# Kernel optimization log

Hardware: AMD Instinct MI355X
Metric: run time of the kernel (lower is better)

Reference implementation:

```python
import jax, jax.numpy as jnp
import numpy as np

WS = 2048            # window_size
STEP = WS // 2       # hop = window_size // 2
NC = WS // 2 + 1     # rfft coeffs
NB = 4               # n_blocks


def _hann():
    # periodic hann window (torch.hann_window default)
    return 0.5 - 0.5 * jnp.cos(2.0 * jnp.pi * jnp.arange(WS) / WS)


def _block(x, transfer, gain):
    # x: (b, 1, time); transfer: (NC,); gain: scalar
    b, ch, time = x.shape
    frames = time // STEP
    padded = jnp.pad(x, ((0, 0), (0, 0), (0, STEP)))
    idx = jnp.arange(frames)[:, None] * STEP + jnp.arange(WS)[None, :]
    windowed = padded[:, :, idx]                       # (b, ch, F, WS)
    spec = jnp.fft.rfft(windowed, axis=-1)             # (b, ch, F, NC) complex
    spec_t = jnp.moveaxis(spec, 2, 0)                  # (F, b, ch, NC)
    tc = transfer.astype(spec.dtype)

    # linear recurrence: out_i = transfer * (spec_i + out_{i-1})
    def step_fn(carry, s):
        out = (s + carry) * tc
        return out, out

    _, outs = jax.lax.scan(step_fn, jnp.zeros_like(spec_t[0]), spec_t)
    wins = jnp.fft.irfft(outs, n=WS, axis=-1) * _hann()  # (F, b, ch, WS)
    wins = jnp.moveaxis(wins, 0, 2)                      # (b, ch, F, WS)
    # overlap-add with hop = WS/2: split each frame into two halves
    first = wins[..., :STEP].reshape(b, ch, frames * STEP)
    second = wins[..., STEP:].reshape(b, ch, frames * STEP)
    samples = (jnp.pad(first, ((0, 0), (0, 0), (0, STEP)))
               + jnp.pad(second, ((0, 0), (0, 0), (STEP, 0))))
    return jnp.tanh(samples * gain)[..., :time]


def setup_inputs() -> dict:
    key = jax.random.key(0)
    k_x, k_b, k_s, k_g = jax.random.split(key, 4)
    x = jax.random.normal(k_x, (32, 1, 262144), dtype=jnp.float32)
    # init_transfer: sparse resonances * scaling * pitch^2
    resonances = (jax.random.uniform(k_b, (NB, NC)) < 0.01).astype(jnp.float32)
    scaling = jax.random.uniform(k_s, (NB, NC), minval=0.9, maxval=0.998)
    pitch = jnp.linspace(1.0, 0.0, NC) ** 2
    transfers = resonances * scaling * pitch[None, :]
    gains = jax.random.uniform(k_g, (NB,), minval=10.0, maxval=200.0)
    mixer = jnp.zeros((NB + 1,), dtype=jnp.float32)
    return {"x": x, "transfers": transfers, "gains": gains, "mixer": mixer}


def reference(x, transfers, gains, mixer):
    outputs = [x]
    inp = x
    for i in range(NB):
        inp = _block(inp, transfers[i], gains[i])
        outputs.append(inp)
    stacked = jnp.stack(outputs, axis=-1)          # (b, 1, time, NB+1)
    mixer_values = jax.nn.softmax(mixer)
    return jnp.sum(stacked * mixer_values, axis=-1)
```

## Files before the change

kernel.cpp:

```cpp
#include <hip/hip_runtime.h>
#include <math.h>
#include <stdint.h>

#define NB   4
#define NC   1025
#define WSZ  2048
#define STEP 1024
#define FRM  256
#define BAT  32
#define TT   262144
#define KC   32
#define YPAD 68

#define RREV (1.0f / 2048.0f)

typedef float f2 __attribute__((ext_vector_type(2)));

__device__ __forceinline__ float tanh_fast(float z) {
    float e = __expf(2.0f * z);
    return 1.0f - 2.0f / (e + 1.0f);
}

__device__ __forceinline__ void cis_rev(int idx, float* c, float* s) {
    float rev = (float)(idx & 2047) * RREV;
    *c = __builtin_amdgcn_cosf(rev);
    *s = __builtin_amdgcn_sinf(rev);
}

__global__ __launch_bounds__(1024) void setup_kernel(
    const float* __restrict__ transfers, const float* __restrict__ mixer,
    int* __restrict__ counts, int* __restrict__ bins, float* __restrict__ tvals,
    float* __restrict__ wmix, float* __restrict__ hann, int kmax)
{
    int i = blockIdx.x, tid = threadIdx.x;
    __shared__ int wcnt[16], woff[16];
    if (i == 0) {
        float cc, ss; cis_rev(tid, &cc, &ss);
        hann[tid] = 0.5f - 0.5f * cc;
    }
    float tv = transfers[i * NC + tid];
    bool nz = (tv != 0.0f);
    unsigned long long mask = __ballot(nz);
    int lane = tid & 63, w = tid >> 6;
    int within = __popcll(mask & ((1ULL << lane) - 1ULL));
    if (lane == 0) wcnt[w] = __popcll(mask);
    __syncthreads();
    if (tid == 0) {
        int acc = 0;
        for (int q = 0; q < 16; ++q) { woff[q] = acc; acc += wcnt[q]; }
        float tvL = transfers[i * NC + 1024];
        if (tvL != 0.0f && acc < kmax) { bins[i * NC + acc] = 1024; tvals[i * NC + acc] = tvL; acc++; }
        counts[i] = (acc < kmax) ? acc : kmax;
        if (i == 0) {
            float m = mixer[0];
            for (int q = 1; q < 5; ++q) m = fmaxf(m, mixer[q]);
            float e[5], s = 0.f;
            for (int q = 0; q < 5; ++q) { e[q] = __expf(mixer[q] - m); s += e[q]; }
            for (int q = 0; q < 5; ++q) wmix[q] = e[q] / s;
        }
    }
    __syncthreads();
    if (nz) {
        int pos = woff[w] + within;
        if (pos < kmax) { bins[i * NC + pos] = tid; tvals[i * NC + pos] = tv; }
    }
}

__global__ __launch_bounds__(256) void table_kernel(
    const int* __restrict__ counts, const int* __restrict__ bins,
    float2* __restrict__ cisA, float2* __restrict__ cisB, int kmax)
{
    int i = blockIdx.x >> 2, c = blockIdx.x & 3;
    int K = counts[i];
    int tid = threadIdx.x;
    for (int j = c; j < K; j += 4) {
        int k = bins[i * NC + j];
        if (tid < 64) {
            float cc, ss; cis_rev(k * tid, &cc, &ss);
            cisA[((size_t)i * kmax + j) * 64 + tid] = make_float2(cc, ss);
        } else if (tid < 80) {
            int q = tid - 64;
            float cc, ss; cis_rev(k * 64 * q, &cc, &ss);
            cisB[((size_t)i * kmax + j) * 16 + q] = make_float2(cc, ss);
        }
    }
}

__device__ __forceinline__ void half_dft(
    const float xr[16], int K, const float2* __restrict__ cA,
    const float2* __restrict__ cB, float2* __restrict__ Hout, int lane, int w)
{
    for (int j = w; j < K; j += 8) {
        int j2 = j + 4;
        bool two = (j2 < K);
        float2 bA = cB[(size_t)j * 16 + 1];
        float2 bB = two ? cB[(size_t)j2 * 16 + 1] : bA;
        float2 wAl = cA[(size_t)j * 64 + lane];
        float2 wBl = two ? cA[(size_t)j2 * 64 + lane] : wAl;
        f2 Wr, Wi, nWi;
        Wr.x = bA.x; Wr.y = bB.x;
        Wi.x = -bA.y; Wi.y = -bB.y;
        nWi = -Wi;
        f2 hr = 0.f, hi = 0.f;
#pragma unroll
        for (int i = 15; i >= 0; --i) {
            f2 xx; xx.x = xr[i]; xx.y = xr[i];
            f2 tmp = nWi * hi + xx;
            f2 nr = Wr * hr + tmp;
            hi = Wi * hr + Wr * hi;
            hr = nr;
        }
        f2 wlc, wls;
        wlc.x = wAl.x; wlc.y = wBl.x;
        wls.x = wAl.y; wls.y = wBl.y;
        f2 re = hr * wlc + hi * wls;
        f2 im = hi * wlc - hr * wls;
        float reA = re.x, imA = im.x, reB = re.y, imB = im.y;
#pragma unroll
        for (int m = 32; m >= 1; m >>= 1) {
            reA += __shfl_xor(reA, m, 64);
            imA += __shfl_xor(imA, m, 64);
            reB += __shfl_xor(reB, m, 64);
            imB += __shfl_xor(imB, m, 64);
        }
        if (lane == 0) {
            Hout[j] = make_float2(reA, imA);
            if (two) Hout[j2] = make_float2(reB, imB);
        }
    }
}

__global__ __launch_bounds__(256, 8) void analysis_kernel(
    const float* __restrict__ x, const int* __restrict__ counts,
    const float2* __restrict__ cisA, const float2* __restrict__ cisB,
    float2* __restrict__ H, int iblk, int kmax)
{
    int wg = blockIdx.x;
    int b = wg >> 8, h = wg & 255;
    int tid = threadIdx.x;
    int lane = tid & 63, w = tid >> 6;
    int K = counts[iblk];
    const float* xb = x + (size_t)b * TT + (size_t)h * STEP;
    float xr[16];
#pragma unroll
    for (int i = 0; i < 16; ++i) xr[i] = xb[lane + (i << 6)];
    const float2* cA = cisA + (size_t)iblk * kmax * 64;
    const float2* cB = cisB + (size_t)iblk * kmax * 16;
    float2* Hout = H + (size_t)(b * FRM + h) * K;
    half_dft(xr, K, cA, cB, Hout, lane, w);
}

__global__ __launch_bounds__(256) void scan_kernel(
    float2* __restrict__ S, const int* __restrict__ counts,
    const int* __restrict__ bins, const float* __restrict__ tvals, int iblk)
{
    int K = counts[iblk];
    int wg = blockIdx.x;
    int b = wg & (BAT - 1), j0 = wg >> 5;
    int f = threadIdx.x;
    int lane = f & 63, w = f >> 6;
    __shared__ float2 wtot[4];
    for (int j = j0; j < K; j += 32) {
        float t = tvals[iblk * NC + j];
        int k = bins[iblk * NC + j];
        float2* Sb = S + (size_t)b * FRM * K + j;
        float2 h1 = Sb[(size_t)f * K];
        float2 h2 = (f < FRM - 1) ? Sb[(size_t)(f + 1) * K] : make_float2(0.f, 0.f);
        float sgn = (k & 1) ? -t : t;
        float ax = fmaf(sgn, h2.x, h1.x * t);
        float ay = fmaf(sgn, h2.y, h1.y * t);
        float td = t;
        float tp0, tp1, tp2, tp3, tp4, tp5;
#pragma unroll
        for (int s = 0; s < 6; ++s) {
            int d = 1 << s;
            if (s == 0) tp0 = td; else if (s == 1) tp1 = td; else if (s == 2) tp2 = td;
            else if (s == 3) tp3 = td; else if (s == 4) tp4 = td; else tp5 = td;
            float bx = __shfl_up(ax, d, 64);
            float by = __shfl_up(ay, d, 64);
            if (lane >= d) { ax = fmaf(td, bx, ax); ay = fmaf(td, by, ay); }
            td *= td;
        }
        if (lane == 63) wtot[w] = make_float2(ax, ay);
        __syncthreads();
        float px = 0.f, py = 0.f;
#pragma unroll
        for (int w2 = 0; w2 < 3; ++w2) {
            if (w2 < w) {
                float2 v = wtot[w2];
                px = fmaf(px, td, v.x);
                py = fmaf(py, td, v.y);
            }
        }
        int n = lane + 1;
        float fac = (n & 64) ? td : 1.0f;
        if (n & 1)  fac *= tp0;
        if (n & 2)  fac *= tp1;
        if (n & 4)  fac *= tp2;
        if (n & 8)  fac *= tp3;
        if (n & 16) fac *= tp4;
        if (n & 32) fac *= tp5;
        ax = fmaf(fac, px, ax);
        ay = fmaf(fac, py, ay);
        Sb[(size_t)f * K] = make_float2(ax, ay);
        __syncthreads();
    }
}

__device__ __forceinline__ void acc4(
    f2& q0, f2& q1, f2& q2, f2& q3, float4 e, float4 a0, float4 a1)
{
    f2 up; up.x = e.x; up.y = e.y;
    f2 vp; vp.x = e.z; vp.y = e.w;
    q0 = up * a0.x + q0; q0 = vp * a0.y + q0;
    q1 = up * a0.z + q1; q1 = vp * a0.w + q1;
    q2 = up * a1.x + q2; q2 = vp * a1.y + q2;
    q3 = up * a1.z + q3; q3 = vp * a1.w + q3;
}

__global__ __launch_bounds__(256, 6) void fused_synth_kernel(
    const float2* __restrict__ S, float2* __restrict__ H2,
    const float2* __restrict__ cisA, const float2* __restrict__ cisB,
    const int* __restrict__ counts, const int* __restrict__ bins,
    const float* __restrict__ gains, const float* __restrict__ wmix,
    const float* __restrict__ hann, const float* __restrict__ x,
    float* __restrict__ dout, int iblk, int do_an, int kmax)
{
    __shared__ float4 smem[1024];
    float4* rc = smem;
    float*  ystage = (float*)smem;
    float4* part = smem + 544;

    int wg = blockIdx.x;
    int b = wg >> 7, s0 = (wg & 127) << 1;
    int tid = threadIdx.x;
    int n1 = tid << 2;
    int q = tid >> 4;
    int m = (tid & 15) << 2;

    int K = counts[iblk];
    const int* bl = bins + iblk * NC;
    const float2* Ob = S + (size_t)b * FRM * K;
    const float2* cA0 = cisA + (size_t)iblk * kmax * 64;
    const float2* cB0 = cisB + (size_t)iblk * kmax * 16;

    f2 p0 = 0.f, p1 = 0.f, p2 = 0.f, p3 = 0.f;
    f2 r0 = 0.f, r1 = 0.f, r2 = 0.f, r3 = 0.f;

    for (int c0 = 0; c0 < K; c0 += KC) {
        int cs = (K - c0 < KC) ? (K - c0) : KC;
        {
            int flat = tid >> 2;
            int seg = flat >> 5;
            int j = flat & 31;
            int jj = c0 + ((j < cs) ? j : (cs - 1));
            int q0 = (tid & 3) << 2;
            int k = bl[jj];
            float g = ((k == 0) || (k == 1024)) ? (1.0f / 2048.0f) : (2.0f / 2048.0f);
            float sg = (k & 1) ? -g : g;
            int fc = s0 + seg;
            float2 o1 = Ob[(size_t)fc * K + jj];
            float2 om = (fc > 0) ? Ob[(size_t)(fc - 1) * K + jj] : make_float2(0.f, 0.f);
            float c2r = om.x * sg, c2i = om.y * sg;
            f2 u; u.x = c2r;  u.y = o1.x * g - c2r;
            f2 v; v.x = -c2i; v.y = -(o1.y * g - c2i);
            const float2* bqp = cB0 + (size_t)jj * 16 + q0;
#pragma unroll
            for (int e = 0; e < 4; ++e) {
                float2 bq = bqp[e];
                f2 up = u * bq.x + v * bq.y;
                f2 vp = v * bq.x - u * bq.y;
                rc[(flat << 4) + q0 + e] = make_float4(up.x, up.y, vp.x, vp.y);
            }
        }
        __syncthreads();
        const float2* cAj = cA0 + ((size_t)c0 << 6) + m;
        const float4* rcq = rc + q;
        int jj = 0;
        for (; jj + 2 <= cs; jj += 2) {
            float4 a00 = *(const float4*)(cAj);
            float4 a01 = *(const float4*)(cAj + 2);
            float4 a10 = *(const float4*)(cAj + 64);
            float4 a11 = *(const float4*)(cAj + 66);
            cAj += 128;
            float4 e00 = rcq[jj << 4];
            float4 e01 = rcq[(KC + jj) << 4];
            float4 e10 = rcq[(jj + 1) << 4];
            float4 e11 = rcq[(KC + jj + 1) << 4];
            acc4(p0, p1, p2, p3, e00, a00, a01);
            acc4(r0, r1, r2, r3, e01, a00, a01);
            acc4(p0, p1, p2, p3, e10, a10, a11);
            acc4(r0, r1, r2, r3, e11, a10, a11);
        }
        if (jj < cs) {
            float4 a0 = *(const float4*)(cAj);
            float4 a1 = *(const float4*)(cAj + 2);
            float4 e0 = rcq[jj << 4];
            float4 e1 = rcq[(KC + jj) << 4];
            acc4(p0, p1, p2, p3, e0, a0, a1);
            acc4(r0, r1, r2, r3, e1, a0, a1);
        }
        __syncthreads();
    }

    size_t base0 = (size_t)b * TT + ((size_t)s0 << 10) + (size_t)n1;
    const float* prevsrc = (iblk == 0) ? x : dout;
    float4 pv0 = *(const float4*)(prevsrc + base0);
    float4 pv1 = *(const float4*)(prevsrc + base0 + 1024);
    float4 hv = *(const float4*)(hann + n1);
    float gain = gains[iblk];
    float wsel = (iblk == 0) ? wmix[0] : 1.0f;
    float wn = wmix[iblk + 1];

    float4 yv0, yv1;
    yv0.x = tanh_fast(fmaf(hv.x, p0.y, p0.x) * gain);
    yv0.y = tanh_fast(fmaf(hv.y, p1.y, p1.x) * gain);
    yv0.z = tanh_fast(fmaf(hv.z, p2.y, p2.x) * gain);
    yv0.w = tanh_fast(fmaf(hv.w, p3.y, p3.x) * gain);
    yv1.x = tanh_fast(fmaf(hv.x, r0.y, r0.x) * gain);
    yv1.y = tanh_fast(fmaf(hv.y, r1.y, r1.x) * gain);
    yv1.z = tanh_fast(fmaf(hv.z, r2.y, r2.x) * gain);
    yv1.w = tanh_fast(fmaf(hv.w, r3.y, r3.x) * gain);

    float4 dv0, dv1;
    dv0.x = fmaf(wsel, pv0.x, wn * yv0.x);
    dv0.y = fmaf(wsel, pv0.y, wn * yv0.y);
    dv0.z = fmaf(wsel, pv0.z, wn * yv0.z);
    dv0.w = fmaf(wsel, pv0.w, wn * yv0.w);
    dv1.x = fmaf(wsel, pv1.x, wn * yv1.x);
    dv1.y = fmaf(wsel, pv1.y, wn * yv1.y);
    dv1.z = fmaf(wsel, pv1.z, wn * yv1.z);
    dv1.w = fmaf(wsel, pv1.w, wn * yv1.w);
    *(float4*)(dout + base0) = dv0;
    *(float4*)(dout + base0 + 1024) = dv1;

    if (do_an) {
        int cw = n1 >> 6, off = n1 & 63;
        *(float4*)(ystage + cw * YPAD + off) = yv0;
        *(float4*)(ystage + 16 * YPAD + cw * YPAD + off) = yv1;
        __syncthreads();
        int K2 = counts[iblk + 1];
        if (K2 > 0) {
            const float2* cA2 = cisA + (size_t)(iblk + 1) * kmax * 64;
            const float2* cB2 = cisB + (size_t)(iblk + 1) * kmax * 16;
            int jloc = tid & 15, c = tid >> 4;
            int lane = tid & 63, wv = tid >> 6;
            const float4* yp0 = (const float4*)(ystage + c * YPAD);
            const float4* yp1 = (const float4*)(ystage + 16 * YPAD + c * YPAD);
            for (int jb = 0; jb < K2; jb += 16) {
                int j = jb + jloc;
                int js = (j < K2) ? j : (K2 - 1);
                float2 w1 = cA2[(size_t)js * 64 + 1];
                float Wr = w1.x, Wi = -w1.y, nWi = w1.y;
                f2 hr = 0.f, hi = 0.f;
#pragma unroll
                for (int i4 = 15; i4 >= 0; --i4) {
                    float4 ya = yp0[i4];
                    float4 yb = yp1[i4];
                    { f2 yy; yy.x = ya.w; yy.y = yb.w;
                      f2 t = hi * nWi + yy; f2 nr = hr * Wr + t; hi = hr * Wi + hi * Wr; hr = nr; }
                    { f2 yy; yy.x = ya.z; yy.y = yb.z;
                      f2 t = hi * nWi + yy; f2 nr = hr * Wr + t; hi = hr * Wi + hi * Wr; hr = nr; }
                    { f2 yy; yy.x = ya.y; yy.y = yb.y;
                      f2 t = hi * nWi + yy; f2 nr = hr * Wr + t; hi = hr * Wi + hi * Wr; hr = nr; }
                    { f2 yy; yy.x = ya.x; yy.y = yb.x;
                      f2 t = hi * nWi + yy; f2 nr = hr * Wr + t; hi = hr * Wi + hi * Wr; hr = nr; }
                }
                float2 bq = cB2[(size_t)js * 16 + c];
                f2 re = hr * bq.x + hi * bq.y;
                f2 im = hi * bq.x - hr * bq.y;
                float4 pr = make_float4(re.x, im.x, re.y, im.y);
                pr.x += __shfl_xor(pr.x, 16, 64);
                pr.y += __shfl_xor(pr.y, 16, 64);
                pr.z += __shfl_xor(pr.z, 16, 64);
                pr.w += __shfl_xor(pr.w, 16, 64);
                pr.x += __shfl_xor(pr.x, 32, 64);
                pr.y += __shfl_xor(pr.y, 32, 64);
                pr.z += __shfl_xor(pr.z, 32, 64);
                pr.w += __shfl_xor(pr.w, 32, 64);
                if (lane < 16) part[wv * 16 + lane] = pr;
                __syncthreads();
                if (tid < 16) {
                    int j2 = jb + tid;
                    if (j2 < K2) {
                        float4 a0 = part[tid];
                        float4 a1 = part[16 + tid];
                        float4 a2 = part[32 + tid];
                        float4 a3 = part[48 + tid];
                        float4 acc;
                        acc.x = (a0.x + a1.x) + (a2.x + a3.x);
                        acc.y = (a0.y + a1.y) + (a2.y + a3.y);
                        acc.z = (a0.z + a1.z) + (a2.z + a3.z);
                        acc.w = (a0.w + a1.w) + (a2.w + a3.w);
                        H2[(size_t)(b * FRM + s0) * K2 + j2] = make_float2(acc.x, acc.y);
                        H2[(size_t)(b * FRM + s0 + 1) * K2 + j2] = make_float2(acc.z, acc.w);
                    }
                }
                __syncthreads();
            }
        }
    }
}

extern "C" void kernel_launch(void* const* d_in, const int* in_sizes, int n_in,
                              void* d_out, int out_size, void* d_ws, size_t ws_size,
                              hipStream_t stream)
{
    const float* x         = (const float*)d_in[0];
    const float* transfers = (const float*)d_in[1];
    const float* gains     = (const float*)d_in[2];
    const float* mixer     = (const float*)d_in[3];
    float* dout = (float*)d_out;

    uint8_t* ws = (uint8_t*)d_ws;
    int*   counts = (int*)ws;
    int*   bins   = (int*)(ws + 64);
    float* tvals  = (float*)(ws + 64 + 16400);
    float* wmix   = (float*)(ws + 64 + 16400 + 16400);
    float* hann   = (float*)(ws + 36864);
    const size_t HDR = 65536;

    long long perk = 2LL * BAT * FRM * 8 + (long long)NB * 80 * 8;
    long long km = ((long long)ws_size - (long long)HDR) / perk;
    int kmax = (int)((km < 1) ? 1 : ((km > NC) ? NC : km));
    float2* S0 = (float2*)(ws + HDR);
    float2* S1 = S0 + (size_t)BAT * FRM * kmax;
    float2* cisA = S1 + (size_t)BAT * FRM * kmax;
    float2* cisB = cisA + (size_t)NB * kmax * 64;

    setup_kernel<<<NB, 1024, 0, stream>>>(transfers, mixer, counts, bins, tvals, wmix, hann, kmax);
    table_kernel<<<NB * 4, 256, 0, stream>>>(counts, bins, cisA, cisB, kmax);
    analysis_kernel<<<BAT * FRM, 256, 0, stream>>>(x, counts, cisA, cisB, S0, 0, kmax);

    float2* cur = S0;
    float2* nxt = S1;
    for (int i = 0; i < NB; ++i) {
        scan_kernel<<<BAT * 32, 256, 0, stream>>>(cur, counts, bins, tvals, i);
        fused_synth_kernel<<<BAT * 128, 256, 0, stream>>>(cur, nxt, cisA, cisB, counts, bins,
                                                          gains, wmix, hann, x, dout, i,
                                                          (i < NB - 1) ? 1 : 0, kmax);
        float2* t = cur; cur = nxt; nxt = t;
    }
}
```

Measured before the change: 240.3 us.

## Process four output segments per workgroup to reuse cis table loads

Each workgroup of the fused synthesis kernel now produces four 1024-sample segments instead of two, so every loaded cisA coefficient is applied to four frames. The chunk size KC is halved so the staged coefficient buffer still fits in shared memory, which grows slightly. The analysis half runs two interleaved Horner recurrences with a combined reduction, cutting the grid to half as many workgroups. The cost is twice the accumulator registers, occupancy hints lowered from 6 to 5, and fewer workgroups to spread across the GPU.

```diff
diff --git a/kernel.cpp b/kernel.cpp
--- a/kernel.cpp
+++ b/kernel.cpp
@@ -9,7 +9,8 @@
 #define FRM  256
 #define BAT  32
 #define TT   262144
-#define KC   32
+#define SEGS 4
+#define KC   16
 #define YPAD 68
 
 #define RREV (1.0f / 2048.0f)
@@ -218,7 +219,7 @@
     q3 = up * a1.z + q3; q3 = vp * a1.w + q3;
 }
 
-__global__ __launch_bounds__(256, 6) void fused_synth_kernel(
+__global__ __launch_bounds__(256, 5) void fused_synth_kernel(
     const float2* __restrict__ S, float2* __restrict__ H2,
     const float2* __restrict__ cisA, const float2* __restrict__ cisB,
     const int* __restrict__ counts, const int* __restrict__ bins,
@@ -226,13 +227,13 @@
     const float* __restrict__ hann, const float* __restrict__ x,
     float* __restrict__ dout, int iblk, int do_an, int kmax)
 {
-    __shared__ float4 smem[1024];
+    __shared__ float4 smem[1216];
     float4* rc = smem;
     float*  ystage = (float*)smem;
-    float4* part = smem + 544;
+    float4* part = smem + 1088;
 
     int wg = blockIdx.x;
-    int b = wg >> 7, s0 = (wg & 127) << 1;
+    int b = wg >> 6, s0 = (wg & 63) << 2;
     int tid = threadIdx.x;
     int n1 = tid << 2;
     int q = tid >> 4;
@@ -244,15 +245,17 @@
     const float2* cA0 = cisA + (size_t)iblk * kmax * 64;
     const float2* cB0 = cisB + (size_t)iblk * kmax * 16;
 
-    f2 p0 = 0.f, p1 = 0.f, p2 = 0.f, p3 = 0.f;
-    f2 r0 = 0.f, r1 = 0.f, r2 = 0.f, r3 = 0.f;
+    f2 p00 = 0.f, p01 = 0.f, p02 = 0.f, p03 = 0.f;
+    f2 p10 = 0.f, p11 = 0.f, p12 = 0.f, p13 = 0.f;
+    f2 p20 = 0.f, p21 = 0.f, p22 = 0.f, p23 = 0.f;
+    f2 p30 = 0.f, p31 = 0.f, p32 = 0.f, p33 = 0.f;
 
     for (int c0 = 0; c0 < K; c0 += KC) {
         int cs = (K - c0 < KC) ? (K - c0) : KC;
         {
             int flat = tid >> 2;
-            int seg = flat >> 5;
-            int j = flat & 31;
+            int seg = flat >> 4;
+            int j = flat & 15;
             int jj = c0 + ((j < cs) ? j : (cs - 1));
             int q0 = (tid & 3) << 2;
             int k = bl[jj];
@@ -283,61 +286,78 @@
             float4 a10 = *(const float4*)(cAj + 64);
             float4 a11 = *(const float4*)(cAj + 66);
             cAj += 128;
-            float4 e00 = rcq[jj << 4];
-            float4 e01 = rcq[(KC + jj) << 4];
-            float4 e10 = rcq[(jj + 1) << 4];
-            float4 e11 = rcq[(KC + jj + 1) << 4];
-            acc4(p0, p1, p2, p3, e00, a00, a01);
-            acc4(r0, r1, r2, r3, e01, a00, a01);
-            acc4(p0, p1, p2, p3, e10, a10, a11);
-            acc4(r0, r1, r2, r3, e11, a10, a11);
+            {
+                float4 e0 = rcq[(0 * KC + jj) << 4];
+                float4 e1 = rcq[(0 * KC + jj + 1) << 4];
+                acc4(p00, p01, p02, p03, e0, a00, a01);
+                acc4(p00, p01, p02, p03, e1, a10, a11);
+            }
+            {
+                float4 e0 = rcq[(1 * KC + jj) << 4];
+                float4 e1 = rcq[(1 * KC + jj + 1) << 4];
+                acc4(p10, p11, p12, p13, e0, a00, a01);
+                acc4(p10, p11, p12, p13, e1, a10, a11);
+            }
+            {
+                float4 e0 = rcq[(2 * KC + jj) << 4];
+                float4 e1 = rcq[(2 * KC + jj + 1) << 4];
+                acc4(p20, p21, p22, p23, e0, a00, a01);
+                acc4(p20, p21, p22, p23, e1, a10, a11);
+            }
+            {
+                float4 e0 = rcq[(3 * KC + jj) << 4];
+                float4 e1 = rcq[(3 * KC + jj + 1) << 4];
+                acc4(p30, p31, p32, p33, e0, a00, a01);
+                acc4(p30, p31, p32, p33, e1, a10, a11);
+            }
         }
         if (jj < cs) {
             float4 a0 = *(const float4*)(cAj);
             float4 a1 = *(const float4*)(cAj + 2);
-            float4 e0 = rcq[jj << 4];
-            float4 e1 = rcq[(KC + jj) << 4];
-            acc4(p0, p1, p2, p3, e0, a0, a1);
-            acc4(r0, r1, r2, r3, e1, a0, a1);
+            float4 e0 = rcq[(0 * KC + jj) << 4];
+            float4 e1 = rcq[(1 * KC + jj) << 4];
+            float4 e2 = rcq[(2 * KC + jj) << 4];
+            float4 e3 = rcq[(3 * KC + jj) << 4];
+            acc4(p00, p01, p02, p03, e0, a0, a1);
+            acc4(p10, p11, p12, p13, e1, a0, a1);
+            acc4(p20, p21, p22, p23, e2, a0, a1);
+            acc4(p30, p31, p32, p33, e3, a0, a1);
         }
         __syncthreads();
     }
 
     size_t base0 = (size_t)b * TT + ((size_t)s0 << 10) + (size_t)n1;
     const float* prevsrc = (iblk == 0) ? x : dout;
-    float4 pv0 = *(const float4*)(prevsrc + base0);
-    float4 pv1 = *(const float4*)(prevsrc + base0 + 1024);
     float4 hv = *(const float4*)(hann + n1);
     float gain = gains[iblk];
     float wsel = (iblk == 0) ? wmix[0] : 1.0f;
     float wn = wmix[iblk + 1];
-
-    float4 yv0, yv1;
-    yv0.x = tanh_fast(fmaf(hv.x, p0.y, p0.x) * gain);
-    yv0.y = tanh_fast(fmaf(hv.y, p1.y, p1.x) * gain);
-    yv0.z = tanh_fast(fmaf(hv.z, p2.y, p2.x) * gain);
-    yv0.w = tanh_fast(fmaf(hv.w, p3.y, p3.x) * gain);
-    yv1.x = tanh_fast(fmaf(hv.x, r0.y, r0.x) * gain);
-    yv1.y = tanh_fast(fmaf(hv.y, r1.y, r1.x) * gain);
-    yv1.z = tanh_fast(fmaf(hv.z, r2.y, r2.x) * gain);
-    yv1.w = tanh_fast(fmaf(hv.w, r3.y, r3.x) * gain);
-
-    float4 dv0, dv1;
-    dv0.x = fmaf(wsel, pv0.x, wn * yv0.x);
-    dv0.y = fmaf(wsel, pv0.y, wn * yv0.y);
-    dv0.z = fmaf(wsel, pv0.z, wn * yv0.z);
-    dv0.w = fmaf(wsel, pv0.w, wn * yv0.w);
-    dv1.x = fmaf(wsel, pv1.x, wn * yv1.x);
-    dv1.y = fmaf(wsel, pv1.y, wn * yv1.y);
-    dv1.z = fmaf(wsel, pv1.z, wn * yv1.z);
-    dv1.w = fmaf(wsel, pv1.w, wn * yv1.w);
-    *(float4*)(dout + base0) = dv0;
-    *(float4*)(dout + base0 + 1024) = dv1;
+    int cw = n1 >> 6, off = n1 & 63;
+
+#define SEG_EPI(s, A0, A1, A2, A3)                                              \
+    {                                                                           \
+        float4 pv = *(const float4*)(prevsrc + base0 + ((size_t)(s) << 10));    \
+        float4 yv;                                                              \
+        yv.x = tanh_fast(fmaf(hv.x, A0.y, A0.x) * gain);                        \
+        yv.y = tanh_fast(fmaf(hv.y, A1.y, A1.x) * gain);                        \
+        yv.z = tanh_fast(fmaf(hv.z, A2.y, A2.x) * gain);                        \
+        yv.w = tanh_fast(fmaf(hv.w, A3.y, A3.x) * gain);                        \
+        float4 dv;                                                              \
+        dv.x = fmaf(wsel, pv.x, wn * yv.x);                                     \
+        dv.y = fmaf(wsel, pv.y, wn * yv.y);                                     \
+        dv.z = fmaf(wsel, pv.z, wn * yv.z);                                     \
+        dv.w = fmaf(wsel, pv.w, wn * yv.w);                                     \
+        *(float4*)(dout + base0 + ((size_t)(s) << 10)) = dv;                    \
+        if (do_an) *(float4*)(ystage + (s) * 16 * YPAD + cw * YPAD + off) = yv; \
+    }
+
+    SEG_EPI(0, p00, p01, p02, p03)
+    SEG_EPI(1, p10, p11, p12, p13)
+    SEG_EPI(2, p20, p21, p22, p23)
+    SEG_EPI(3, p30, p31, p32, p33)
+#undef SEG_EPI
 
     if (do_an) {
-        int cw = n1 >> 6, off = n1 & 63;
-        *(float4*)(ystage + cw * YPAD + off) = yv0;
-        *(float4*)(ystage + 16 * YPAD + cw * YPAD + off) = yv1;
         __syncthreads();
         int K2 = counts[iblk + 1];
         if (K2 > 0) {
@@ -347,53 +367,73 @@
             int lane = tid & 63, wv = tid >> 6;
             const float4* yp0 = (const float4*)(ystage + c * YPAD);
             const float4* yp1 = (const float4*)(ystage + 16 * YPAD + c * YPAD);
+            const float4* yp2 = (const float4*)(ystage + 32 * YPAD + c * YPAD);
+            const float4* yp3 = (const float4*)(ystage + 48 * YPAD + c * YPAD);
             for (int jb = 0; jb < K2; jb += 16) {
                 int j = jb + jloc;
                 int js = (j < K2) ? j : (K2 - 1);
                 float2 w1 = cA2[(size_t)js * 64 + 1];
                 float Wr = w1.x, Wi = -w1.y, nWi = w1.y;
-                f2 hr = 0.f, hi = 0.f;
+                f2 hrA = 0.f, hiA = 0.f;
+                f2 hrB = 0.f, hiB = 0.f;
 #pragma unroll
                 for (int i4 = 15; i4 >= 0; --i4) {
                     float4 ya = yp0[i4];
                     float4 yb = yp1[i4];
-                    { f2 yy; yy.x = ya.w; yy.y = yb.w;
-                      f2 t = hi * nWi + yy; f2 nr = hr * Wr + t; hi = hr * Wi + hi * Wr; hr = nr; }
-                    { f2 yy; yy.x = ya.z; yy.y = yb.z;
-                      f2 t = hi * nWi + yy; f2 nr = hr * Wr + t; hi = hr * Wi + hi * Wr; hr = nr; }
-                    { f2 yy; yy.x = ya.y; yy.y = yb.y;
-                      f2 t = hi * nWi + yy; f2 nr = hr * Wr + t; hi = hr * Wi + hi * Wr; hr = nr; }
-                    { f2 yy; yy.x = ya.x; yy.y = yb.x;
-                      f2 t = hi * nWi + yy; f2 nr = hr * Wr + t; hi = hr * Wi + hi * Wr; hr = nr; }
+                    float4 yc = yp2[i4];
+                    float4 yd = yp3[i4];
+#define HSTEP(CC)                                                                   \
+                    { f2 yy; yy.x = ya.CC; yy.y = yb.CC;                            \
+                      f2 t = hiA * nWi + yy; f2 nr = hrA * Wr + t;                  \
+                      hiA = hrA * Wi + hiA * Wr; hrA = nr; }                        \
+                    { f2 yy; yy.x = yc.CC; yy.y = yd.CC;                            \
+                      f2 t = hiB * nWi + yy; f2 nr = hrB * Wr + t;                  \
+                      hiB = hrB * Wi + hiB * Wr; hrB = nr; }
+                    HSTEP(w)
+                    HSTEP(z)
+                    HSTEP(y)
+                    HSTEP(x)
+#undef HSTEP
                 }
                 float2 bq = cB2[(size_t)js * 16 + c];
-                f2 re = hr * bq.x + hi * bq.y;
-                f2 im = hi * bq.x - hr * bq.y;
-                float4 pr = make_float4(re.x, im.x, re.y, im.y);
-                pr.x += __shfl_xor(pr.x, 16, 64);
-                pr.y += __shfl_xor(pr.y, 16, 64);
-                pr.z += __shfl_xor(pr.z, 16, 64);
-                pr.w += __shfl_xor(pr.w, 16, 64);
-                pr.x += __shfl_xor(pr.x, 32, 64);
-                pr.y += __shfl_xor(pr.y, 32, 64);
-                pr.z += __shfl_xor(pr.z, 32, 64);
-                pr.w += __shfl_xor(pr.w, 32, 64);
-                if (lane < 16) part[wv * 16 + lane] = pr;
+                f2 reA = hrA * bq.x + hiA * bq.y;
+                f2 imA = hiA * bq.x - hrA * bq.y;
+                f2 reB = hrB * bq.x + hiB * bq.y;
+                f2 imB = hiB * bq.x - hrB * bq.y;
+                float4 prA = make_float4(reA.x, imA.x, reA.y, imA.y);
+                float4 prB = make_float4(reB.x, imB.x, reB.y, imB.y);
+#pragma unroll
+                for (int d = 16; d <= 32; d <<= 1) {
+                    prA.x += __shfl_xor(prA.x, d, 64);
+                    prA.y += __shfl_xor(prA.y, d, 64);
+                    prA.z += __shfl_xor(prA.z, d, 64);
+                    prA.w += __shfl_xor(prA.w, d, 64);
+                    prB.x += __shfl_xor(prB.x, d, 64);
+                    prB.y += __shfl_xor(prB.y, d, 64);
+                    prB.z += __shfl_xor(prB.z, d, 64);
+                    prB.w += __shfl_xor(prB.w, d, 64);
+                }
+                if (lane < 16) {
+                    part[wv * 16 + lane] = prA;
+                    part[64 + wv * 16 + lane] = prB;
+                }
                 __syncthreads();
-                if (tid < 16) {
-                    int j2 = jb + tid;
+                if (tid < 32) {
+                    int sel = tid >> 4, t = tid & 15;
+                    int j2 = jb + t;
                     if (j2 < K2) {
-                        float4 a0 = part[tid];
-                        float4 a1 = part[16 + tid];
-                        float4 a2 = part[32 + tid];
-                        float4 a3 = part[48 + tid];
+                        const float4* pp = part + sel * 64;
+                        float4 a0 = pp[t];
+                        float4 a1 = pp[16 + t];
+                        float4 a2 = pp[32 + t];
+                        float4 a3 = pp[48 + t];
                         float4 acc;
                         acc.x = (a0.x + a1.x) + (a2.x + a3.x);
                         acc.y = (a0.y + a1.y) + (a2.y + a3.y);
                         acc.z = (a0.z + a1.z) + (a2.z + a3.z);
                         acc.w = (a0.w + a1.w) + (a2.w + a3.w);
-                        H2[(size_t)(b * FRM + s0) * K2 + j2] = make_float2(acc.x, acc.y);
-                        H2[(size_t)(b * FRM + s0 + 1) * K2 + j2] = make_float2(acc.z, acc.w);
+                        H2[(size_t)(b * FRM + s0 + sel * 2) * K2 + j2] = make_float2(acc.x, acc.y);
+                        H2[(size_t)(b * FRM + s0 + sel * 2 + 1) * K2 + j2] = make_float2(acc.z, acc.w);
                     }
                 }
                 __syncthreads();
@@ -436,9 +476,9 @@
     float2* nxt = S1;
     for (int i = 0; i < NB; ++i) {
         scan_kernel<<<BAT * 32, 256, 0, stream>>>(cur, counts, bins, tvals, i);
-        fused_synth_kernel<<<BAT * 128, 256, 0, stream>>>(cur, nxt, cisA, cisB, counts, bins,
-                                                          gains, wmix, hann, x, dout, i,
-                                                          (i < NB - 1) ? 1 : 0, kmax);
+        fused_synth_kernel<<<BAT * (FRM / SEGS), 256, 0, stream>>>(cur, nxt, cisA, cisB, counts, bins,
+                                                                   gains, wmix, hann, x, dout, i,
+                                                                   (i < NB - 1) ? 1 : 0, kmax);
         float2* t = cur; cur = nxt; nxt = t;
     }
 }
```

New measurement: 234.2 us. 1.03x faster.

## Map one wave per frame half, drop LDS and barriers in analysis and synthesis

Applied to the files above, without the earlier changes.

Analysis and fused synthesis now assign one 64-lane wave to each half-frame, with each lane owning 16 contiguous samples. Synthesis broadcasts per-bin coefficients with readlane and generates twiddles by rotation recurrence in registers, replacing the LDS-staged chunked accumulation and its barriers. The next block's analysis reuses the same wave-level DFT directly from register-held outputs. This cuts shared-memory traffic and synchronisation, at the cost of more registers (16 complex accumulators), rotation rounding drift and more redundant per-wave loads.

```diff
diff --git a/kernel.cpp b/kernel.cpp
--- a/kernel.cpp
+++ b/kernel.cpp
@@ -9,8 +9,6 @@
 #define FRM  256
 #define BAT  32
 #define TT   262144
-#define KC   32
-#define YPAD 68
 
 #define RREV (1.0f / 2048.0f)
 
@@ -25,6 +23,10 @@
     float rev = (float)(idx & 2047) * RREV;
     *c = __builtin_amdgcn_cosf(rev);
     *s = __builtin_amdgcn_sinf(rev);
+}
+
+__device__ __forceinline__ float rl(float v, int l) {
+    return __int_as_float(__builtin_amdgcn_readlane(__float_as_int(v), l));
 }
 
 __global__ __launch_bounds__(1024) void setup_kernel(
@@ -86,68 +88,76 @@
     }
 }
 
-__device__ __forceinline__ void half_dft(
-    const float xr[16], int K, const float2* __restrict__ cA,
-    const float2* __restrict__ cB, float2* __restrict__ Hout, int lane, int w)
-{
-    for (int j = w; j < K; j += 8) {
-        int j2 = j + 4;
+__device__ __forceinline__ void wave_dft16(
+    const float y[16], int K, const float2* __restrict__ cA,
+    const float2* __restrict__ cB, float2* __restrict__ Hout, int lane)
+{
+    int la = (lane & 3) << 4, lb = lane >> 2;
+    for (int j = 0; j < K; j += 2) {
+        int j2 = j + 1;
         bool two = (j2 < K);
-        float2 bA = cB[(size_t)j * 16 + 1];
-        float2 bB = two ? cB[(size_t)j2 * 16 + 1] : bA;
-        float2 wAl = cA[(size_t)j * 64 + lane];
-        float2 wBl = two ? cA[(size_t)j2 * 64 + lane] : wAl;
+        float2 w1A = cA[(size_t)j * 64 + 1];
+        float2 w1B = two ? cA[(size_t)j2 * 64 + 1] : w1A;
         f2 Wr, Wi, nWi;
-        Wr.x = bA.x; Wr.y = bB.x;
-        Wi.x = -bA.y; Wi.y = -bB.y;
+        Wr.x = w1A.x; Wr.y = w1B.x;
+        Wi.x = -w1A.y; Wi.y = -w1B.y;
         nWi = -Wi;
         f2 hr = 0.f, hi = 0.f;
 #pragma unroll
-        for (int i = 15; i >= 0; --i) {
-            f2 xx; xx.x = xr[i]; xx.y = xr[i];
-            f2 tmp = nWi * hi + xx;
+        for (int r = 15; r >= 0; --r) {
+            f2 yy; yy.x = y[r]; yy.y = y[r];
+            f2 tmp = nWi * hi + yy;
             f2 nr = Wr * hr + tmp;
             hi = Wi * hr + Wr * hi;
             hr = nr;
         }
-        f2 wlc, wls;
-        wlc.x = wAl.x; wlc.y = wBl.x;
-        wls.x = wAl.y; wls.y = wBl.y;
-        f2 re = hr * wlc + hi * wls;
-        f2 im = hi * wlc - hr * wls;
-        float reA = re.x, imA = im.x, reB = re.y, imB = im.y;
-#pragma unroll
-        for (int m = 32; m >= 1; m >>= 1) {
-            reA += __shfl_xor(reA, m, 64);
-            imA += __shfl_xor(imA, m, 64);
-            reB += __shfl_xor(reB, m, 64);
-            imB += __shfl_xor(imB, m, 64);
+        float2 aA = cA[(size_t)j * 64 + la];
+        float2 bA = cB[(size_t)j * 16 + lb];
+        float2 aB = two ? cA[(size_t)j2 * 64 + la] : aA;
+        float2 bB = two ? cB[(size_t)j2 * 16 + lb] : bA;
+        f2 zx, zy;
+        zx.x = aA.x * bA.x - aA.y * bA.y;
+        zy.x = aA.x * bA.y + aA.y * bA.x;
+        zx.y = aB.x * bB.x - aB.y * bB.y;
+        zy.y = aB.x * bB.y + aB.y * bB.x;
+        f2 re = hr * zx + hi * zy;
+        f2 im = hi * zx - hr * zy;
+        float r0 = re.x, r1 = re.y, i0 = im.x, i1 = im.y;
+#pragma unroll
+        for (int d = 32; d >= 1; d >>= 1) {
+            r0 += __shfl_xor(r0, d, 64);
+            i0 += __shfl_xor(i0, d, 64);
+            r1 += __shfl_xor(r1, d, 64);
+            i1 += __shfl_xor(i1, d, 64);
         }
         if (lane == 0) {
-            Hout[j] = make_float2(reA, imA);
-            if (two) Hout[j2] = make_float2(reB, imB);
-        }
-    }
-}
-
-__global__ __launch_bounds__(256, 8) void analysis_kernel(
+            Hout[j] = make_float2(r0, i0);
+            if (two) Hout[j2] = make_float2(r1, i1);
+        }
+    }
+}
+
+__global__ __launch_bounds__(256) void analysis_kernel(
     const float* __restrict__ x, const int* __restrict__ counts,
     const float2* __restrict__ cisA, const float2* __restrict__ cisB,
-    float2* __restrict__ H, int iblk, int kmax)
-{
-    int wg = blockIdx.x;
-    int b = wg >> 8, h = wg & 255;
-    int tid = threadIdx.x;
-    int lane = tid & 63, w = tid >> 6;
-    int K = counts[iblk];
-    const float* xb = x + (size_t)b * TT + (size_t)h * STEP;
-    float xr[16];
-#pragma unroll
-    for (int i = 0; i < 16; ++i) xr[i] = xb[lane + (i << 6)];
-    const float2* cA = cisA + (size_t)iblk * kmax * 64;
-    const float2* cB = cisB + (size_t)iblk * kmax * 16;
-    float2* Hout = H + (size_t)(b * FRM + h) * K;
-    half_dft(xr, K, cA, cB, Hout, lane, w);
+    float2* __restrict__ H, int kmax)
+{
+    int gw = (blockIdx.x << 2) + (threadIdx.x >> 6);
+    int lane = threadIdx.x & 63;
+    int b = gw >> 8, h = gw & 255;
+    int K = counts[0];
+    if (K <= 0) return;
+    const float* xb = x + (size_t)b * TT + (size_t)h * STEP + ((size_t)lane << 4);
+    float y[16];
+    float4 q0 = *(const float4*)(xb);
+    float4 q1 = *(const float4*)(xb + 4);
+    float4 q2 = *(const float4*)(xb + 8);
+    float4 q3 = *(const float4*)(xb + 12);
+    y[0] = q0.x;  y[1] = q0.y;  y[2] = q0.z;  y[3] = q0.w;
+    y[4] = q1.x;  y[5] = q1.y;  y[6] = q1.z;  y[7] = q1.w;
+    y[8] = q2.x;  y[9] = q2.y;  y[10] = q2.z; y[11] = q2.w;
+    y[12] = q3.x; y[13] = q3.y; y[14] = q3.z; y[15] = q3.w;
+    wave_dft16(y, K, cisA, cisB, H + (size_t)(b * FRM + h) * K, lane);
 }
 
 __global__ __launch_bounds__(256) void scan_kernel(
@@ -207,18 +217,7 @@
     }
 }
 
-__device__ __forceinline__ void acc4(
-    f2& q0, f2& q1, f2& q2, f2& q3, float4 e, float4 a0, float4 a1)
-{
-    f2 up; up.x = e.x; up.y = e.y;
-    f2 vp; vp.x = e.z; vp.y = e.w;
-    q0 = up * a0.x + q0; q0 = vp * a0.y + q0;
-    q1 = up * a0.z + q1; q1 = vp * a0.w + q1;
-    q2 = up * a1.x + q2; q2 = vp * a1.y + q2;
-    q3 = up * a1.z + q3; q3 = vp * a1.w + q3;
-}
-
-__global__ __launch_bounds__(256, 6) void fused_synth_kernel(
+__global__ __launch_bounds__(256, 5) void fused_synth_kernel(
     const float2* __restrict__ S, float2* __restrict__ H2,
     const float2* __restrict__ cisA, const float2* __restrict__ cisB,
     const int* __restrict__ counts, const int* __restrict__ bins,
@@ -226,178 +225,90 @@
     const float* __restrict__ hann, const float* __restrict__ x,
     float* __restrict__ dout, int iblk, int do_an, int kmax)
 {
-    __shared__ float4 smem[1024];
-    float4* rc = smem;
-    float*  ystage = (float*)smem;
-    float4* part = smem + 544;
-
-    int wg = blockIdx.x;
-    int b = wg >> 7, s0 = (wg & 127) << 1;
-    int tid = threadIdx.x;
-    int n1 = tid << 2;
-    int q = tid >> 4;
-    int m = (tid & 15) << 2;
+    int gw = (blockIdx.x << 2) + (threadIdx.x >> 6);
+    int lane = threadIdx.x & 63;
+    int b = gw >> 8, s = gw & 255;
 
     int K = counts[iblk];
     const int* bl = bins + iblk * NC;
     const float2* Ob = S + (size_t)b * FRM * K;
     const float2* cA0 = cisA + (size_t)iblk * kmax * 64;
     const float2* cB0 = cisB + (size_t)iblk * kmax * 16;
-
-    f2 p0 = 0.f, p1 = 0.f, p2 = 0.f, p3 = 0.f;
-    f2 r0 = 0.f, r1 = 0.f, r2 = 0.f, r3 = 0.f;
-
-    for (int c0 = 0; c0 < K; c0 += KC) {
-        int cs = (K - c0 < KC) ? (K - c0) : KC;
-        {
-            int flat = tid >> 2;
-            int seg = flat >> 5;
-            int j = flat & 31;
-            int jj = c0 + ((j < cs) ? j : (cs - 1));
-            int q0 = (tid & 3) << 2;
-            int k = bl[jj];
-            float g = ((k == 0) || (k == 1024)) ? (1.0f / 2048.0f) : (2.0f / 2048.0f);
-            float sg = (k & 1) ? -g : g;
-            int fc = s0 + seg;
-            float2 o1 = Ob[(size_t)fc * K + jj];
-            float2 om = (fc > 0) ? Ob[(size_t)(fc - 1) * K + jj] : make_float2(0.f, 0.f);
-            float c2r = om.x * sg, c2i = om.y * sg;
-            f2 u; u.x = c2r;  u.y = o1.x * g - c2r;
-            f2 v; v.x = -c2i; v.y = -(o1.y * g - c2i);
-            const float2* bqp = cB0 + (size_t)jj * 16 + q0;
-#pragma unroll
-            for (int e = 0; e < 4; ++e) {
-                float2 bq = bqp[e];
-                f2 up = u * bq.x + v * bq.y;
-                f2 vp = v * bq.x - u * bq.y;
-                rc[(flat << 4) + q0 + e] = make_float4(up.x, up.y, vp.x, vp.y);
+    int la = (lane & 3) << 4, lb = lane >> 2;
+
+    f2 acc[16];
+#pragma unroll
+    for (int r = 0; r < 16; ++r) acc[r] = 0.f;
+
+    for (int jb = 0; jb < K; jb += 64) {
+        int nj = K - jb; if (nj > 64) nj = 64;
+        int jl = jb + ((lane < nj) ? lane : (nj - 1));
+        int k = bl[jl];
+        float g = ((k == 0) || (k == 1024)) ? (1.0f / 2048.0f) : (2.0f / 2048.0f);
+        float sg = (k & 1) ? -g : g;
+        float2 o1 = Ob[(size_t)s * K + jl];
+        float2 om = (s > 0) ? Ob[(size_t)(s - 1) * K + jl] : make_float2(0.f, 0.f);
+        float c2r = om.x * sg, c2i = om.y * sg;
+        float uxl = c2r;
+        float uyl = o1.x * g - c2r;
+        float vxl = -c2i;
+        float vyl = c2i - o1.y * g;
+        float2 rtl = cA0[(size_t)jl * 64 + 1];
+
+        for (int jo = 0; jo < nj; ++jo) {
+            int j = jb + jo;
+            float ux = rl(uxl, jo), uy = rl(uyl, jo);
+            float vx = rl(vxl, jo), vy = rl(vyl, jo);
+            float rc = rl(rtl.x, jo), rs = rl(rtl.y, jo);
+            float2 a  = cA0[(size_t)j * 64 + la];
+            float2 bq = cB0[(size_t)j * 16 + lb];
+            float zx = a.x * bq.x - a.y * bq.y;
+            float zy = a.x * bq.y + a.y * bq.x;
+            f2 uu; uu.x = ux; uu.y = uy;
+            f2 vv; vv.x = vx; vv.y = vy;
+#pragma unroll
+            for (int r = 0; r < 16; ++r) {
+                acc[r] = uu * zx + acc[r];
+                acc[r] = vv * zy + acc[r];
+                float nzx = fmaf(zx, rc, -(zy * rs));
+                zy = fmaf(zx, rs, zy * rc);
+                zx = nzx;
             }
         }
-        __syncthreads();
-        const float2* cAj = cA0 + ((size_t)c0 << 6) + m;
-        const float4* rcq = rc + q;
-        int jj = 0;
-        for (; jj + 2 <= cs; jj += 2) {
-            float4 a00 = *(const float4*)(cAj);
-            float4 a01 = *(const float4*)(cAj + 2);
-            float4 a10 = *(const float4*)(cAj + 64);
-            float4 a11 = *(const float4*)(cAj + 66);
-            cAj += 128;
-            float4 e00 = rcq[jj << 4];
-            float4 e01 = rcq[(KC + jj) << 4];
-            float4 e10 = rcq[(jj + 1) << 4];
-            float4 e11 = rcq[(KC + jj + 1) << 4];
-            acc4(p0, p1, p2, p3, e00, a00, a01);
-            acc4(r0, r1, r2, r3, e01, a00, a01);
-            acc4(p0, p1, p2, p3, e10, a10, a11);
-            acc4(r0, r1, r2, r3, e11, a10, a11);
-        }
-        if (jj < cs) {
-            float4 a0 = *(const float4*)(cAj);
-            float4 a1 = *(const float4*)(cAj + 2);
-            float4 e0 = rcq[jj << 4];
-            float4 e1 = rcq[(KC + jj) << 4];
-            acc4(p0, p1, p2, p3, e0, a0, a1);
-            acc4(r0, r1, r2, r3, e1, a0, a1);
-        }
-        __syncthreads();
-    }
-
-    size_t base0 = (size_t)b * TT + ((size_t)s0 << 10) + (size_t)n1;
+    }
+
+    size_t base = (size_t)b * TT + ((size_t)s << 10) + ((size_t)lane << 4);
     const float* prevsrc = (iblk == 0) ? x : dout;
-    float4 pv0 = *(const float4*)(prevsrc + base0);
-    float4 pv1 = *(const float4*)(prevsrc + base0 + 1024);
-    float4 hv = *(const float4*)(hann + n1);
+    const float* hb = hann + (lane << 4);
     float gain = gains[iblk];
     float wsel = (iblk == 0) ? wmix[0] : 1.0f;
     float wn = wmix[iblk + 1];
-
-    float4 yv0, yv1;
-    yv0.x = tanh_fast(fmaf(hv.x, p0.y, p0.x) * gain);
-    yv0.y = tanh_fast(fmaf(hv.y, p1.y, p1.x) * gain);
-    yv0.z = tanh_fast(fmaf(hv.z, p2.y, p2.x) * gain);
-    yv0.w = tanh_fast(fmaf(hv.w, p3.y, p3.x) * gain);
-    yv1.x = tanh_fast(fmaf(hv.x, r0.y, r0.x) * gain);
-    yv1.y = tanh_fast(fmaf(hv.y, r1.y, r1.x) * gain);
-    yv1.z = tanh_fast(fmaf(hv.z, r2.y, r2.x) * gain);
-    yv1.w = tanh_fast(fmaf(hv.w, r3.y, r3.x) * gain);
-
-    float4 dv0, dv1;
-    dv0.x = fmaf(wsel, pv0.x, wn * yv0.x);
-    dv0.y = fmaf(wsel, pv0.y, wn * yv0.y);
-    dv0.z = fmaf(wsel, pv0.z, wn * yv0.z);
-    dv0.w = fmaf(wsel, pv0.w, wn * yv0.w);
-    dv1.x = fmaf(wsel, pv1.x, wn * yv1.x);
-    dv1.y = fmaf(wsel, pv1.y, wn * yv1.y);
-    dv1.z = fmaf(wsel, pv1.z, wn * yv1.z);
-    dv1.w = fmaf(wsel, pv1.w, wn * yv1.w);
-    *(float4*)(dout + base0) = dv0;
-    *(float4*)(dout + base0 + 1024) = dv1;
+    float y[16];
+#pragma unroll
+    for (int c = 0; c < 4; ++c) {
+        float4 hv = *(const float4*)(hb + (c << 2));
+        float4 pv = *(const float4*)(prevsrc + base + (c << 2));
+        float y0 = tanh_fast(fmaf(hv.x, acc[(c << 2) + 0].y, acc[(c << 2) + 0].x) * gain);
+        float y1 = tanh_fast(fmaf(hv.y, acc[(c << 2) + 1].y, acc[(c << 2) + 1].x) * gain);
+        float y2 = tanh_fast(fmaf(hv.z, acc[(c << 2) + 2].y, acc[(c << 2) + 2].x) * gain);
+        float y3 = tanh_fast(fmaf(hv.w, acc[(c << 2) + 3].y, acc[(c << 2) + 3].x) * gain);
+        y[(c << 2) + 0] = y0; y[(c << 2) + 1] = y1;
+        y[(c << 2) + 2] = y2; y[(c << 2) + 3] = y3;
+        float4 dv;
+        dv.x = fmaf(wsel, pv.x, wn * y0);
+        dv.y = fmaf(wsel, pv.y, wn * y1);
+        dv.z = fmaf(wsel, pv.z, wn * y2);
+        dv.w = fmaf(wsel, pv.w, wn * y3);
+        *(float4*)(dout + base + (c << 2)) = dv;
+    }
 
     if (do_an) {
-        int cw = n1 >> 6, off = n1 & 63;
-        *(float4*)(ystage + cw * YPAD + off) = yv0;
-        *(float4*)(ystage + 16 * YPAD + cw * YPAD + off) = yv1;
-        __syncthreads();
         int K2 = counts[iblk + 1];
         if (K2 > 0) {
-            const float2* cA2 = cisA + (size_t)(iblk + 1) * kmax * 64;
-            const float2* cB2 = cisB + (size_t)(iblk + 1) * kmax * 16;
-            int jloc = tid & 15, c = tid >> 4;
-            int lane = tid & 63, wv = tid >> 6;
-            const float4* yp0 = (const float4*)(ystage + c * YPAD);
-            const float4* yp1 = (const float4*)(ystage + 16 * YPAD + c * YPAD);
-            for (int jb = 0; jb < K2; jb += 16) {
-                int j = jb + jloc;
-                int js = (j < K2) ? j : (K2 - 1);
-                float2 w1 = cA2[(size_t)js * 64 + 1];
-                float Wr = w1.x, Wi = -w1.y, nWi = w1.y;
-                f2 hr = 0.f, hi = 0.f;
-#pragma unroll
-                for (int i4 = 15; i4 >= 0; --i4) {
-                    float4 ya = yp0[i4];
-                    float4 yb = yp1[i4];
-                    { f2 yy; yy.x = ya.w; yy.y = yb.w;
-                      f2 t = hi * nWi + yy; f2 nr = hr * Wr + t; hi = hr * Wi + hi * Wr; hr = nr; }
-                    { f2 yy; yy.x = ya.z; yy.y = yb.z;
-                      f2 t = hi * nWi + yy; f2 nr = hr * Wr + t; hi = hr * Wi + hi * Wr; hr = nr; }
-                    { f2 yy; yy.x = ya.y; yy.y = yb.y;
-                      f2 t = hi * nWi + yy; f2 nr = hr * Wr + t; hi = hr * Wi + hi * Wr; hr = nr; }
-                    { f2 yy; yy.x = ya.x; yy.y = yb.x;
-                      f2 t = hi * nWi + yy; f2 nr = hr * Wr + t; hi = hr * Wi + hi * Wr; hr = nr; }
-                }
-                float2 bq = cB2[(size_t)js * 16 + c];
-                f2 re = hr * bq.x + hi * bq.y;
-                f2 im = hi * bq.x - hr * bq.y;
-                float4 pr = make_float4(re.x, im.x, re.y, im.y);
-                pr.x += __shfl_xor(pr.x, 16, 64);
-                pr.y += __shfl_xor(pr.y, 16, 64);
-                pr.z += __shfl_xor(pr.z, 16, 64);
-                pr.w += __shfl_xor(pr.w, 16, 64);
-                pr.x += __shfl_xor(pr.x, 32, 64);
-                pr.y += __shfl_xor(pr.y, 32, 64);
-                pr.z += __shfl_xor(pr.z, 32, 64);
-                pr.w += __shfl_xor(pr.w, 32, 64);
-                if (lane < 16) part[wv * 16 + lane] = pr;
-                __syncthreads();
-                if (tid < 16) {
-                    int j2 = jb + tid;
-                    if (j2 < K2) {
-                        float4 a0 = part[tid];
-                        float4 a1 = part[16 + tid];
-                        float4 a2 = part[32 + tid];
-                        float4 a3 = part[48 + tid];
-                        float4 acc;
-                        acc.x = (a0.x + a1.x) + (a2.x + a3.x);
-                        acc.y = (a0.y + a1.y) + (a2.y + a3.y);
-                        acc.z = (a0.z + a1.z) + (a2.z + a3.z);
-                        acc.w = (a0.w + a1.w) + (a2.w + a3.w);
-                        H2[(size_t)(b * FRM + s0) * K2 + j2] = make_float2(acc.x, acc.y);
-                        H2[(size_t)(b * FRM + s0 + 1) * K2 + j2] = make_float2(acc.z, acc.w);
-                    }
-                }
-                __syncthreads();
-            }
+            wave_dft16(y, K2,
+                       cisA + (size_t)(iblk + 1) * kmax * 64,
+                       cisB + (size_t)(iblk + 1) * kmax * 16,
+                       H2 + (size_t)(b * FRM + s) * K2, lane);
         }
     }
 }
@@ -430,15 +341,15 @@
 
     setup_kernel<<<NB, 1024, 0, stream>>>(transfers, mixer, counts, bins, tvals, wmix, hann, kmax);
     table_kernel<<<NB * 4, 256, 0, stream>>>(counts, bins, cisA, cisB, kmax);
-    analysis_kernel<<<BAT * FRM, 256, 0, stream>>>(x, counts, cisA, cisB, S0, 0, kmax);
+    analysis_kernel<<<BAT * FRM / 4, 256, 0, stream>>>(x, counts, cisA, cisB, S0, kmax);
 
     float2* cur = S0;
     float2* nxt = S1;
     for (int i = 0; i < NB; ++i) {
         scan_kernel<<<BAT * 32, 256, 0, stream>>>(cur, counts, bins, tvals, i);
-        fused_synth_kernel<<<BAT * 128, 256, 0, stream>>>(cur, nxt, cisA, cisB, counts, bins,
-                                                          gains, wmix, hann, x, dout, i,
-                                                          (i < NB - 1) ? 1 : 0, kmax);
+        fused_synth_kernel<<<BAT * FRM / 4, 256, 0, stream>>>(cur, nxt, cisA, cisB, counts, bins,
+                                                              gains, wmix, hann, x, dout, i,
+                                                              (i < NB - 1) ? 1 : 0, kmax);
         float2* t = cur; cur = nxt; nxt = t;
     }
 }
```

Result: slower. 287.0 us (+19.4%).
